# Kernel optimization log

Hardware: AMD Instinct MI355X
Metric: run time of the kernel (lower is better)

The kernel has to match this reference:

```python
import jax, jax.numpy as jnp
import numpy as np

B, C, H, W = 64, 3, 256, 256
K = 2  # multi_n_num
EPS_NORM = 1e-8
EPS_DEN = 1e-7
SCALE = 0.01


def setup_inputs() -> dict:
    key = jax.random.key(0)
    ka, kp, kn, kj = jax.random.split(key, 4)
    a = jax.random.normal(ka, (B, C, H, W), dtype=jnp.float32)
    p = jax.random.normal(kp, (B, C, H, W), dtype=jnp.float32)
    n = jax.random.normal(kn, (B, C, H, W), dtype=jnp.float32)
    # sample_with_j(B, 2, i) -> [i, random j != i]
    ar = jnp.arange(B, dtype=jnp.int64)
    off = jax.random.randint(kj, (B,), 1, B)  # offset in [1, B) guarantees j != i
    neg_idx = jnp.stack([ar, (ar + off) % B], axis=1).astype(jnp.int64)  # [B, K]
    return {"a": a, "p": p, "n": n, "neg_idx": neg_idx}


def _fft_norm(x):
    # torch.fft.fft2 over last two dims -> complex, same rank as x
    f = jnp.fft.fft2(x, axes=(-2, -1))  # [B, C, H, W] complex64
    # torch.norm(f, p=2, dim=1, keepdim=True) on complex = sqrt(sum |f|^2 over C)
    nrm = jnp.sqrt(jnp.sum(jnp.abs(f) ** 2, axis=1, keepdims=True))
    return f / (nrm + EPS_NORM) * SCALE


def reference(a, p, n, neg_idx):
    af = _fft_norm(a)
    pf = _fft_norm(p)
    nf = _fft_norm(n)
    # L1Loss on complex tensors = mean |diff| (complex magnitude)
    d_ap = jnp.mean(jnp.abs(af - pf), axis=(1, 2, 3))  # [B]
    n_sel = nf[neg_idx]  # [B, K, C, H, W]
    d_an = jnp.mean(jnp.abs(af[:, None] - n_sel), axis=(2, 3, 4))  # [B, K]
    contrastive = jnp.sum(d_ap[:, None] / (d_an + EPS_DEN))
    return contrastive / (K * B)
```

## Files before the change

### kernel.cpp

```cpp
#include <hip/hip_runtime.h>
#include <hip/hip_fp16.h>

#define B_ 64
#define SW_ 132
#define SIMG_ (256 * SW_)
#define TIMG_ (3 * SIMG_)
#define TELEMS_ ((size_t)B_ * TIMG_)
#define SST_ 257

typedef unsigned u32;

__device__ __forceinline__ u32 h2add(u32 a, u32 b) {
  __half2 r = __hadd2(__builtin_bit_cast(__half2, a), __builtin_bit_cast(__half2, b));
  return __builtin_bit_cast(u32, r);
}
__device__ __forceinline__ u32 h2sub(u32 a, u32 b) {
  __half2 r = __hsub2(__builtin_bit_cast(__half2, a), __builtin_bit_cast(__half2, b));
  return __builtin_bit_cast(u32, r);
}
__device__ __forceinline__ u32 h2mul(u32 a, u32 b) {
  __half2 r = __hmul2(__builtin_bit_cast(__half2, a), __builtin_bit_cast(__half2, b));
  return __builtin_bit_cast(u32, r);
}
__device__ __forceinline__ u32 h2fma(u32 a, u32 b, u32 c) {
  __half2 r = __hfma2(__builtin_bit_cast(__half2, a), __builtin_bit_cast(__half2, b),
                      __builtin_bit_cast(__half2, c));
  return __builtin_bit_cast(u32, r);
}
__device__ __forceinline__ u32 rot16(u32 u) { return (u >> 16) | (u << 16); }
#define NEG_HI_ 0x80000000u
#define NEG_LO_ 0x00008000u
#define HALF2C_ 0x38003800u

__device__ __forceinline__ u32 cmulh(u32 x, u32 tr, u32 ti) {
  u32 m = h2mul(rot16(x), ti);
  return h2fma(x, tr, m ^ NEG_LO_);
}

__device__ __forceinline__ u32 f2u(float2 v) {
  __half2 h = __float22half2_rn(v);
  return __builtin_bit_cast(u32, h);
}
__device__ __forceinline__ float2 u2f(u32 u) {
  return __half22float2(__builtin_bit_cast(__half2, u));
}
__device__ __forceinline__ float2 cmulf(float2 a, float2 b) {
  return make_float2(a.x * b.x - a.y * b.y, a.x * b.y + a.y * b.x);
}

__device__ __forceinline__ void bfly4h(u32 x[4], const u32* twr, const u32* twi, bool tw) {
  u32 a = h2add(x[0], x[2]);
  u32 b = h2sub(x[0], x[2]);
  u32 c = h2add(x[1], x[3]);
  u32 d = h2sub(x[1], x[3]);
  u32 e = rot16(d);
  u32 y1 = h2add(b, e ^ NEG_HI_);
  u32 y2 = h2sub(a, c);
  u32 y3 = h2add(b, e ^ NEG_LO_);
  x[0] = h2add(a, c);
  if (tw) { y1 = cmulh(y1, twr[0], twi[0]); y2 = cmulh(y2, twr[1], twi[1]);
            y3 = cmulh(y3, twr[2], twi[2]); }
  x[1] = y1; x[2] = y2; x[3] = y3;
}

__device__ __forceinline__ void swap16(u32& A, u32& B) {
  asm("v_permlane16_swap_b32 %0, %1" : "+v"(A), "+v"(B));
}
__device__ __forceinline__ void swap32(u32& A, u32& B) {
  asm("v_permlane32_swap_b32 %0, %1" : "+v"(A), "+v"(B));
}
template <int BIT>
__device__ __forceinline__ void xsel(u32& A, u32& B, int r) {
  bool hi = (r >> BIT) & 1;
  int send = hi ? (int)A : (int)B;
  int got;
  if constexpr (BIT == 0)
    got = __builtin_amdgcn_update_dpp(0, send, 0xB1, 0xF, 0xF, false);
  else if constexpr (BIT == 1)
    got = __builtin_amdgcn_update_dpp(0, send, 0x4E, 0xF, 0xF, false);
  else if constexpr (BIT == 2)
    got = __builtin_amdgcn_ds_swizzle(send, 0x101F);
  else
    got = __builtin_amdgcn_ds_swizzle(send, 0x201F);
  if (hi) A = (u32)got; else B = (u32)got;
}
__device__ __forceinline__ void xdig45(u32 u[4]) {
  swap16(u[0], u[1]);
  swap16(u[2], u[3]);
  swap32(u[0], u[2]);
  swap32(u[1], u[3]);
}
template <int BIT>
__device__ __forceinline__ void xdig(u32 u[4], int r) {
  xsel<BIT>(u[0], u[1], r);
  xsel<BIT>(u[2], u[3], r);
  xsel<BIT + 1>(u[0], u[2], r);
  xsel<BIT + 1>(u[1], u[3], r);
}

template <int NF>
__device__ __forceinline__ void fft256h(u32 (&u)[NF][4], int r,
                                        const u32 twr[9], const u32 twi[9]) {
#pragma unroll
  for (int f = 0; f < NF; ++f) bfly4h(u[f], twr + 0, twi + 0, true);
#pragma unroll
  for (int f = 0; f < NF; ++f) xdig45(u[f]);
#pragma unroll
  for (int f = 0; f < NF; ++f) bfly4h(u[f], twr + 3, twi + 3, true);
#pragma unroll
  for (int f = 0; f < NF; ++f) xdig<2>(u[f], r);
#pragma unroll
  for (int f = 0; f < NF; ++f) bfly4h(u[f], twr + 6, twi + 6, true);
#pragma unroll
  for (int f = 0; f < NF; ++f) xdig<0>(u[f], r);
#pragma unroll
  for (int f = 0; f < NF; ++f) bfly4h(u[f], twr, twi, false);
}

__device__ __forceinline__ void tw_init_h(u32 twr[9], u32 twi[9], int r) {
  float2 t[9];
  float s, c;
  __sincosf(-6.283185307179586f * (float)r / 256.0f, &s, &c);
  t[0] = make_float2(c, s); t[1] = cmulf(t[0], t[0]); t[2] = cmulf(t[1], t[0]);
  __sincosf(-6.283185307179586f * (float)(r & 15) / 64.0f, &s, &c);
  t[3] = make_float2(c, s); t[4] = cmulf(t[3], t[3]); t[5] = cmulf(t[4], t[3]);
  __sincosf(-6.283185307179586f * (float)(r & 3) / 16.0f, &s, &c);
  t[6] = make_float2(c, s); t[7] = cmulf(t[6], t[6]); t[8] = cmulf(t[7], t[6]);
#pragma unroll
  for (int i = 0; i < 9; ++i) {
    u32 hr = (u32)__half_as_ushort(__float2half_rn(t[i].x));
    u32 hi = (u32)__half_as_ushort(__float2half_rn(t[i].y));
    twr[i] = hr | (hr << 16);
    twi[i] = hi | (hi << 16);
  }
}

__global__ __launch_bounds__(1024, 4) void fft2_fused(const float* __restrict__ a,
                                                      const float* __restrict__ p,
                                                      const float* __restrict__ n,
                                                      unsigned* __restrict__ outbase,
                                                      float* __restrict__ acc) {
  __shared__ u32 S[129 * SST_];

  int tid = threadIdx.x;
  int wv = tid >> 6;
  int r = tid & 63;
  int tensor = blockIdx.x / 192;
  int plane = blockIdx.x % 192;
  const float* in = (tensor == 0 ? a : (tensor == 1 ? p : n)) + (size_t)plane * 65536;
  unsigned* outp = outbase + (size_t)tensor * TELEMS_ + (size_t)plane * SIMG_;

  if (blockIdx.x == 0 && tid < 192) acc[tid] = 0.0f;

  u32 twr[9], twi[9];
  tw_init_h(twr, twi, r);
  int m = ((r & 3) << 4) | (((r >> 2) & 3) << 2) | (r >> 4);
  int mp = (64 - m) & 63;
  int rp = ((mp >> 4) & 3) | (((mp >> 2) & 3) << 2) | ((mp & 3) << 4);

  {
    float xs[8][8];
#pragma unroll
    for (int f = 0; f < 8; ++f) {
      int q = wv + 16 * f;
      const float* rw = in + (size_t)(2 * q) * 256;
#pragma unroll
      for (int j = 0; j < 4; ++j) {
        xs[f][2 * j]     = rw[r + 64 * j];
        xs[f][2 * j + 1] = rw[256 + r + 64 * j];
      }
    }
    u32 u[8][4];
#pragma unroll
    for (int f = 0; f < 8; ++f)
#pragma unroll
      for (int j = 0; j < 4; ++j)
        u[f][j] = f2u(make_float2(xs[f][2 * j], xs[f][2 * j + 1]));
    fft256h<8>(u, r, twr, twi);
#pragma unroll
    for (int f = 0; f < 8; ++f) {
      int q = wv + 16 * f;
      u32 m0 = (u32)__shfl((int)u[f][0], rp, 64);
      u32 m2 = (u32)__shfl((int)u[f][2], rp, 64);
      u32 m3 = (u32)__shfl((int)u[f][3], rp, 64);
      u32 Zk0 = u[f][0];
      u32 Zk1 = u[f][1];
      u32 Zm0 = (m == 0) ? m0 : m3;
      u32 Zm1 = (m == 0) ? m3 : m2;
      u32 Aa = h2mul(HALF2C_, h2add(Zk0, Zm0 ^ NEG_HI_));
      u32 Ab = h2mul(HALF2C_, h2add(rot16(Zm0), rot16(Zk0) ^ NEG_HI_));
      u32 Ba = h2mul(HALF2C_, h2add(Zk1, Zm1 ^ NEG_HI_));
      u32 Bb = h2mul(HALF2C_, h2add(rot16(Zm1), rot16(Zk1) ^ NEG_HI_));
      S[m * SST_ + 2 * q]            = Aa;
      S[m * SST_ + 2 * q + 1]        = Ab;
      S[(64 + m) * SST_ + 2 * q]     = Ba;
      S[(64 + m) * SST_ + 2 * q + 1] = Bb;
      if (r == 0) {
        S[128 * SST_ + 2 * q]     = u[f][2] & 0xFFFFu;
        S[128 * SST_ + 2 * q + 1] = u[f][2] >> 16;
      }
    }
  }

  __syncthreads();

  {
    u32 u[8][4];
#pragma unroll
    for (int f = 0; f < 8; ++f) {
      const u32* row = S + (size_t)(wv + 16 * f) * SST_;
#pragma unroll
      for (int j = 0; j < 4; ++j) u[f][j] = row[r + 64 * j];
    }
    fft256h<8>(u, r, twr, twi);
#pragma unroll
    for (int f = 0; f < 8; ++f) {
      int c = wv + 16 * f;
      *(uint4*)(outp + (size_t)c * 256 + 4 * r) =
          make_uint4(u[f][0], u[f][1], u[f][2], u[f][3]);
    }
  }
  if (wv == 0) {
    u32 u1[1][4];
    const u32* srow = S + 128 * SST_;
#pragma unroll
    for (int j = 0; j < 4; ++j) u1[0][j] = srow[r + 64 * j];
    fft256h<1>(u1, r, twr, twi);
    *(uint4*)(outp + (size_t)128 * 256 + 4 * r) =
        make_uint4(u1[0][0], u1[0][1], u1[0][2], u1[0][3]);
  }
  if (wv >= 13) {
    int c = 129 + (wv - 13);
    *(uint4*)(outp + (size_t)c * 256 + 4 * r) = make_uint4(0, 0, 0, 0);
  }
}

__device__ __forceinline__ float cab2(float2 v) { return v.x * v.x + v.y * v.y; }
__device__ __forceinline__ float fsqrt_(float x) { return __builtin_amdgcn_sqrtf(x); }
__device__ __forceinline__ float frcp_(float x) { return __builtin_amdgcn_rcpf(x); }

__global__ __launch_bounds__(256) void dist_kernel(const unsigned* __restrict__ af,
                                                   const unsigned* __restrict__ pf,
                                                   const unsigned* __restrict__ nf,
                                                   const int* __restrict__ neg,
                                                   float* __restrict__ acc) {
  int b = blockIdx.y;
  int j = (neg[1] == 0) ? (int)((const long long*)neg)[b * 2 + 1] : neg[b * 2 + 1];
  size_t ab = (size_t)b * TIMG_;
  size_t jb = (size_t)j * TIMG_;
  int t4 = blockIdx.x * 256 + threadIdx.x;
  int flat0 = t4 * 4;
  int k2 = flat0 >> 8;
  float w = (k2 == 0 || k2 >= 128) ? 1.0f : 2.0f;

  unsigned A[3][4], P[3][4], N[3][4], M[3][4];
#pragma unroll
  for (int ch = 0; ch < 3; ++ch) {
    uint4 t;
    t = *(const uint4*)(af + ab + ch * SIMG_ + flat0); A[ch][0]=t.x; A[ch][1]=t.y; A[ch][2]=t.z; A[ch][3]=t.w;
    t = *(const uint4*)(pf + ab + ch * SIMG_ + flat0); P[ch][0]=t.x; P[ch][1]=t.y; P[ch][2]=t.z; P[ch][3]=t.w;
    t = *(const uint4*)(nf + ab + ch * SIMG_ + flat0); N[ch][0]=t.x; N[ch][1]=t.y; N[ch][2]=t.z; N[ch][3]=t.w;
    t = *(const uint4*)(nf + jb + ch * SIMG_ + flat0); M[ch][0]=t.x; M[ch][1]=t.y; M[ch][2]=t.z; M[ch][3]=t.w;
  }
  float s_ap = 0.0f, s_a0 = 0.0f, s_a1 = 0.0f;
#pragma unroll
  for (int e = 0; e < 4; ++e) {
    float2 a0 = u2f(A[0][e]), a1 = u2f(A[1][e]), a2 = u2f(A[2][e]);
    float2 p0 = u2f(P[0][e]), p1 = u2f(P[1][e]), p2 = u2f(P[2][e]);
    float2 n0 = u2f(N[0][e]), n1 = u2f(N[1][e]), n2 = u2f(N[2][e]);
    float2 m0 = u2f(M[0][e]), m1 = u2f(M[1][e]), m2 = u2f(M[2][e]);
    float sa = 0.01f * frcp_(fsqrt_(cab2(a0) + cab2(a1) + cab2(a2)) + 1e-8f);
    float sp = 0.01f * frcp_(fsqrt_(cab2(p0) + cab2(p1) + cab2(p2)) + 1e-8f);
    float sn = 0.01f * frcp_(fsqrt_(cab2(n0) + cab2(n1) + cab2(n2)) + 1e-8f);
    float sm = 0.01f * frcp_(fsqrt_(cab2(m0) + cab2(m1) + cab2(m2)) + 1e-8f);
    float dx, dy;
    dx = a0.x * sa - p0.x * sp; dy = a0.y * sa - p0.y * sp; s_ap += fsqrt_(dx * dx + dy * dy);
    dx = a1.x * sa - p1.x * sp; dy = a1.y * sa - p1.y * sp; s_ap += fsqrt_(dx * dx + dy * dy);
    dx = a2.x * sa - p2.x * sp; dy = a2.y * sa - p2.y * sp; s_ap += fsqrt_(dx * dx + dy * dy);
    dx = a0.x * sa - n0.x * sn; dy = a0.y * sa - n0.y * sn; s_a0 += fsqrt_(dx * dx + dy * dy);
    dx = a1.x * sa - n1.x * sn; dy = a1.y * sa - n1.y * sn; s_a0 += fsqrt_(dx * dx + dy * dy);
    dx = a2.x * sa - n2.x * sn; dy = a2.y * sa - n2.y * sn; s_a0 += fsqrt_(dx * dx + dy * dy);
    dx = a0.x * sa - m0.x * sm; dy = a0.y * sa - m0.y * sm; s_a1 += fsqrt_(dx * dx + dy * dy);
    dx = a1.x * sa - m1.x * sm; dy = a1.y * sa - m1.y * sm; s_a1 += fsqrt_(dx * dx + dy * dy);
    dx = a2.x * sa - m2.x * sm; dy = a2.y * sa - m2.y * sm; s_a1 += fsqrt_(dx * dx + dy * dy);
  }
  s_ap *= w; s_a0 *= w; s_a1 *= w;
#pragma unroll
  for (int off = 32; off > 0; off >>= 1) {
    s_ap += __shfl_down(s_ap, off);
    s_a0 += __shfl_down(s_a0, off);
    s_a1 += __shfl_down(s_a1, off);
  }
  __shared__ float red[3][4];
  int lane = threadIdx.x & 63, wid = threadIdx.x >> 6;
  if (lane == 0) { red[0][wid] = s_ap; red[1][wid] = s_a0; red[2][wid] = s_a1; }
  __syncthreads();
  if (threadIdx.x == 0) {
    atomicAdd(&acc[b * 3 + 0], red[0][0] + red[0][1] + red[0][2] + red[0][3]);
    atomicAdd(&acc[b * 3 + 1], red[1][0] + red[1][1] + red[1][2] + red[1][3]);
    atomicAdd(&acc[b * 3 + 2], red[2][0] + red[2][1] + red[2][2] + red[2][3]);
  }
}

__global__ void final_kernel(const float* __restrict__ acc, float* __restrict__ out) {
  int b = threadIdx.x;
  const float inv = 1.0f / 196608.0f;
  float dap = acc[b * 3 + 0] * inv;
  float da0 = acc[b * 3 + 1] * inv;
  float da1 = acc[b * 3 + 2] * inv;
  float term = dap / (da0 + 1e-7f) + dap / (da1 + 1e-7f);
#pragma unroll
  for (int off = 32; off > 0; off >>= 1) term += __shfl_down(term, off);
  if (b == 0) out[0] = term * (1.0f / 128.0f);
}

extern "C" void kernel_launch(void* const* d_in, const int* in_sizes, int n_in,
                              void* d_out, int out_size, void* d_ws, size_t ws_size,
                              hipStream_t stream) {
  const float* a = (const float*)d_in[0];
  const float* p = (const float*)d_in[1];
  const float* n = (const float*)d_in[2];
  const int* neg = (const int*)d_in[3];
  float* out = (float*)d_out;

  unsigned* base = (unsigned*)d_ws;
  float* acc = (float*)(base + 3 * TELEMS_);

  fft2_fused<<<576, 1024, 0, stream>>>(a, p, n, base, acc);
  dist_kernel<<<dim3(33, 64), 256, 0, stream>>>(base, base + TELEMS_,
                                                base + 2 * TELEMS_, neg, acc);
  final_kernel<<<1, 64, 0, stream>>>(acc, out);
}
```

Measured before the change: 230.5 us.

## Halve FFT shared-memory buffer by staging column halves in two passes

The fused 2D FFT kernel now holds the second half of the row-FFT spectrum in registers and keeps only the first half in LDS. After the first half is read back it reuses the same buffer for the second half. This roughly halves LDS per block (about 66KB down to about 33KB), and the launch bound is raised to allow twice as many blocks resident. The cost is two extra block barriers, more live registers, and column FFTs run as two batches of four instead of one batch of eight.

```diff
diff --git a/kernel.cpp b/kernel.cpp
--- a/kernel.cpp
+++ b/kernel.cpp
@@ -135,12 +135,12 @@
   }
 }
 
-__global__ __launch_bounds__(1024, 4) void fft2_fused(const float* __restrict__ a,
+__global__ __launch_bounds__(1024, 8) void fft2_fused(const float* __restrict__ a,
                                                       const float* __restrict__ p,
                                                       const float* __restrict__ n,
                                                       unsigned* __restrict__ outbase,
                                                       float* __restrict__ acc) {
-  __shared__ u32 S[129 * SST_];
+  __shared__ u32 S[65 * SST_];
 
   int tid = threadIdx.x;
   int wv = tid >> 6;
@@ -158,24 +158,18 @@
   int mp = (64 - m) & 63;
   int rp = ((mp >> 4) & 3) | (((mp >> 2) & 3) << 2) | ((mp & 3) << 4);
 
+  u32 ba[8], bb[8];
+
   {
-    float xs[8][8];
+    u32 u[8][4];
 #pragma unroll
     for (int f = 0; f < 8; ++f) {
       int q = wv + 16 * f;
       const float* rw = in + (size_t)(2 * q) * 256;
 #pragma unroll
-      for (int j = 0; j < 4; ++j) {
-        xs[f][2 * j]     = rw[r + 64 * j];
-        xs[f][2 * j + 1] = rw[256 + r + 64 * j];
-      }
+      for (int j = 0; j < 4; ++j)
+        u[f][j] = f2u(make_float2(rw[r + 64 * j], rw[256 + r + 64 * j]));
     }
-    u32 u[8][4];
-#pragma unroll
-    for (int f = 0; f < 8; ++f)
-#pragma unroll
-      for (int j = 0; j < 4; ++j)
-        u[f][j] = f2u(make_float2(xs[f][2 * j], xs[f][2 * j + 1]));
     fft256h<8>(u, r, twr, twi);
 #pragma unroll
     for (int f = 0; f < 8; ++f) {
@@ -189,49 +183,74 @@
       u32 Zm1 = (m == 0) ? m3 : m2;
       u32 Aa = h2mul(HALF2C_, h2add(Zk0, Zm0 ^ NEG_HI_));
       u32 Ab = h2mul(HALF2C_, h2add(rot16(Zm0), rot16(Zk0) ^ NEG_HI_));
-      u32 Ba = h2mul(HALF2C_, h2add(Zk1, Zm1 ^ NEG_HI_));
-      u32 Bb = h2mul(HALF2C_, h2add(rot16(Zm1), rot16(Zk1) ^ NEG_HI_));
-      S[m * SST_ + 2 * q]            = Aa;
-      S[m * SST_ + 2 * q + 1]        = Ab;
-      S[(64 + m) * SST_ + 2 * q]     = Ba;
-      S[(64 + m) * SST_ + 2 * q + 1] = Bb;
+      ba[f]  = h2mul(HALF2C_, h2add(Zk1, Zm1 ^ NEG_HI_));
+      bb[f]  = h2mul(HALF2C_, h2add(rot16(Zm1), rot16(Zk1) ^ NEG_HI_));
+      S[m * SST_ + 2 * q]     = Aa;
+      S[m * SST_ + 2 * q + 1] = Ab;
       if (r == 0) {
-        S[128 * SST_ + 2 * q]     = u[f][2] & 0xFFFFu;
-        S[128 * SST_ + 2 * q + 1] = u[f][2] >> 16;
+        S[64 * SST_ + 2 * q]     = u[f][2] & 0xFFFFu;
+        S[64 * SST_ + 2 * q + 1] = u[f][2] >> 16;
       }
     }
   }
 
   __syncthreads();
 
+  u32 uA[4][4];
+#pragma unroll
+  for (int f = 0; f < 4; ++f) {
+    const u32* row = S + (size_t)(wv + 16 * f) * SST_;
+#pragma unroll
+    for (int j = 0; j < 4; ++j) uA[f][j] = row[r + 64 * j];
+  }
+
+  __syncthreads();
+
+#pragma unroll
+  for (int f = 0; f < 8; ++f) {
+    int q = wv + 16 * f;
+    S[m * SST_ + 2 * q]     = ba[f];
+    S[m * SST_ + 2 * q + 1] = bb[f];
+  }
+
+  fft256h<4>(uA, r, twr, twi);
+#pragma unroll
+  for (int f = 0; f < 4; ++f) {
+    int c = wv + 16 * f;
+    *(uint4*)(outp + (size_t)c * 256 + 4 * r) =
+        make_uint4(uA[f][0], uA[f][1], uA[f][2], uA[f][3]);
+  }
+  if (wv >= 13) {
+    int c = 129 + (wv - 13);
+    *(uint4*)(outp + (size_t)c * 256 + 4 * r) = make_uint4(0, 0, 0, 0);
+  }
+
+  __syncthreads();
+
   {
-    u32 u[8][4];
-#pragma unroll
-    for (int f = 0; f < 8; ++f) {
+    u32 uB[4][4];
+#pragma unroll
+    for (int f = 0; f < 4; ++f) {
       const u32* row = S + (size_t)(wv + 16 * f) * SST_;
 #pragma unroll
-      for (int j = 0; j < 4; ++j) u[f][j] = row[r + 64 * j];
+      for (int j = 0; j < 4; ++j) uB[f][j] = row[r + 64 * j];
     }
-    fft256h<8>(u, r, twr, twi);
-#pragma unroll
-    for (int f = 0; f < 8; ++f) {
-      int c = wv + 16 * f;
+    fft256h<4>(uB, r, twr, twi);
+#pragma unroll
+    for (int f = 0; f < 4; ++f) {
+      int c = 64 + wv + 16 * f;
       *(uint4*)(outp + (size_t)c * 256 + 4 * r) =
-          make_uint4(u[f][0], u[f][1], u[f][2], u[f][3]);
+          make_uint4(uB[f][0], uB[f][1], uB[f][2], uB[f][3]);
     }
   }
   if (wv == 0) {
     u32 u1[1][4];
-    const u32* srow = S + 128 * SST_;
+    const u32* srow = S + 64 * SST_;
 #pragma unroll
     for (int j = 0; j < 4; ++j) u1[0][j] = srow[r + 64 * j];
     fft256h<1>(u1, r, twr, twi);
     *(uint4*)(outp + (size_t)128 * 256 + 4 * r) =
         make_uint4(u1[0][0], u1[0][1], u1[0][2], u1[0][3]);
-  }
-  if (wv >= 13) {
-    int c = 129 + (wv - 13);
-    *(uint4*)(outp + (size_t)c * 256 + 4 * r) = make_uint4(0, 0, 0, 0);
   }
 }
 
```

New measurement: 261.8 us. +13.6%, slower.
